# Optimization experiments

Hardware: AMD Instinct MI355X
Metric: run time of the kernel (lower is better)

The kernel has to match this reference:

```python
import jax, jax.numpy as jnp
import numpy as np

N, E = 100000, 1600000
D_IN, D_H, D_OUT = 128, 128, 64


def setup_inputs() -> dict:
    key = jax.random.key(0)
    ks = jax.random.split(key, 9)
    features = jax.random.normal(ks[0], (N, D_IN), dtype=jnp.float32)
    src = jax.random.randint(ks[1], (E,), 0, N, dtype=jnp.int32)
    dst = jax.random.randint(ks[2], (E,), 0, N, dtype=jnp.int32)
    # GraphConv weights (glorot-ish scale)
    W1 = jax.random.normal(ks[3], (D_IN, D_H), dtype=jnp.float32) * (1.0 / np.sqrt(D_IN))
    b1 = jnp.zeros((D_H,), dtype=jnp.float32)
    W2 = jax.random.normal(ks[4], (D_H, D_H), dtype=jnp.float32) * (1.0 / np.sqrt(D_H))
    b2 = jnp.zeros((D_H,), dtype=jnp.float32)
    W3 = jax.random.normal(ks[5], (D_H, D_OUT), dtype=jnp.float32) * (1.0 / np.sqrt(D_H))
    b3 = jnp.zeros((D_OUT,), dtype=jnp.float32)
    return {"features": features, "src": src, "dst": dst,
            "W1": W1, "b1": b1, "W2": W2, "b2": b2, "W3": W3, "b3": b3}


def reference(features, src, dst, W1, b1, W2, b2, W3, b3):
    n = features.shape[0]
    ones_e = jnp.ones(src.shape[0], dtype=features.dtype)
    # DGL GraphConv norm='both': degrees clamped to min 1
    out_deg = jnp.clip(jax.ops.segment_sum(ones_e, src, num_segments=n), 1.0)
    in_deg = jnp.clip(jax.ops.segment_sum(ones_e, dst, num_segments=n), 1.0)
    norm_src = out_deg ** -0.5  # [N]
    norm_dst = in_deg ** -0.5   # [N]

    def graph_conv(h, W, b, relu):
        h = h * norm_src[:, None]                                   # D_out^{-1/2} scale
        m = jax.ops.segment_sum(h[src], dst, num_segments=n)        # SpMM aggregate
        m = m * norm_dst[:, None]                                   # D_in^{-1/2} scale
        h = m @ W + b                                               # linear
        return jax.nn.relu(h) if relu else h

    # dropout is identity in eval mode (deterministic reference)
    h = graph_conv(features, W1, b1, True)
    h = graph_conv(h, W2, b2, True)
    h = graph_conv(h, W3, b3, False)
    return jax.nn.log_softmax(h, axis=1)
```

## Files before the change

### kernel.cpp

```cpp
#include <hip/hip_runtime.h>
#include <math.h>

#define D 128
#define DO 64

#define CHUNK_BITS 15
#define CHUNK_SZ   32768
#define HWORDS     (CHUNK_SZ/4)
#define NSLICE     64

typedef unsigned int uint32;
typedef short bf8s __attribute__((ext_vector_type(8)));
typedef float f32x16 __attribute__((ext_vector_type(16)));

__device__ __forceinline__ unsigned short f2bf(float f) {
    uint32 u = __float_as_uint(f);
    u += 0x7FFFu + ((u >> 16) & 1u);
    return (unsigned short)(u >> 16);
}
__device__ __forceinline__ float bf_lo(uint32 p) { return __uint_as_float(p << 16); }
__device__ __forceinline__ float bf_hi(uint32 p) { return __uint_as_float(p & 0xFFFF0000u); }
__device__ __forceinline__ void acc2(float4& a, uint2 q) {
    a.x += bf_lo(q.x); a.y += bf_hi(q.x);
    a.z += bf_lo(q.y); a.w += bf_hi(q.y);
}
__device__ __forceinline__ void accs(float4& a, uint2 q, float s) {
    a.x = fmaf(bf_lo(q.x), s, a.x); a.y = fmaf(bf_hi(q.x), s, a.y);
    a.z = fmaf(bf_lo(q.y), s, a.z); a.w = fmaf(bf_hi(q.y), s, a.w);
}

__device__ __forceinline__ f32x16 mfma32(bf8s a, bf8s b, f32x16 c) {
    return __builtin_amdgcn_mfma_f32_32x32x16_bf16(a, b, c, 0, 0, 0);
}
#define ZERO16 {0.f,0.f,0.f,0.f,0.f,0.f,0.f,0.f,0.f,0.f,0.f,0.f,0.f,0.f,0.f,0.f}

__global__ void k_pack_w(const float* __restrict__ W1, const float* __restrict__ W2,
                         const float* __restrict__ W3,
                         unsigned short* __restrict__ P1, unsigned short* __restrict__ P2,
                         unsigned short* __restrict__ P3) {
    int t = blockIdx.x * 256 + threadIdx.x;
    const float* W; unsigned short* P; int slot, NCT, ncols;
    if (t < 2048)      { W = W1; P = P1; slot = t;        NCT = 4; ncols = 128; }
    else if (t < 4096) { W = W2; P = P2; slot = t - 2048; NCT = 4; ncols = 128; }
    else if (t < 5120) { W = W3; P = P3; slot = t - 4096; NCT = 2; ncols = 64;  }
    else return;
    int lane = slot & 63, rest = slot >> 6;
    int ct = rest % NCT, ks = rest / NCT;
    int k0 = ks * 16 + (lane >> 5) * 8;
    int colidx = ct * 32 + (lane & 31);
    unsigned u[4];
#pragma unroll
    for (int b = 0; b < 4; ++b) {
        unsigned lo = f2bf(W[(size_t)(k0 + 2 * b) * ncols + colidx]);
        unsigned hi = f2bf(W[(size_t)(k0 + 2 * b + 1) * ncols + colidx]);
        u[b] = lo | (hi << 16);
    }
    ((uint4*)P)[slot] = make_uint4(u[0], u[1], u[2], u[3]);
}

__global__ __launch_bounds__(256) void k_hist_gemm1(
    const int* __restrict__ src, const int* __restrict__ dst, int E,
    int NH, int NBg, int gemmPer,
    uint32* __restrict__ histS, uint32* __restrict__ histD,
    const float* __restrict__ F, const unsigned short* __restrict__ Wp1,
    unsigned short* __restrict__ T1, int N) {
    __shared__ __align__(16) char smemraw[64 * 132 * 4];
    const int tid = threadIdx.x;
    const int P = 1 + gemmPer;
    const int per = blockIdx.x / P;
    const int pos = blockIdx.x % P;

    if (pos == 0) {
        if (per >= 2 * NH) return;
        bool isS = per >= NH;
        int h = isS ? per - NH : per;
        int chunk = h / NSLICE, slice = h % NSLICE;
        const int* key = isS ? src : dst;
        uint32* hist = (uint32*)smemraw;
        for (int w = tid; w < HWORDS; w += 256) hist[w] = 0;
        __syncthreads();
        int base = chunk << CHUNK_BITS;
        const int nE4 = E >> 2;
        int lo = (int)(((long long)slice * nE4) / NSLICE);
        int hi = (int)(((long long)(slice + 1) * nE4) / NSLICE);
        for (int idx = lo + tid; idx < hi; idx += 256) {
            int4 k4 = ((const int4*)key)[idx];
            unsigned o;
            o = (unsigned)(k4.x - base); if (o < CHUNK_SZ) atomicAdd(&hist[o >> 2], 1u << ((o & 3) * 8));
            o = (unsigned)(k4.y - base); if (o < CHUNK_SZ) atomicAdd(&hist[o >> 2], 1u << ((o & 3) * 8));
            o = (unsigned)(k4.z - base); if (o < CHUNK_SZ) atomicAdd(&hist[o >> 2], 1u << ((o & 3) * 8));
            o = (unsigned)(k4.w - base); if (o < CHUNK_SZ) atomicAdd(&hist[o >> 2], 1u << ((o & 3) * 8));
        }
        if (slice == NSLICE - 1 && tid == 0) {
            for (int i = nE4 * 4; i < E; ++i) {
                unsigned o = (unsigned)(key[i] - base);
                if (o < CHUNK_SZ) atomicAdd(&hist[o >> 2], 1u << ((o & 3) * 8));
            }
        }
        __syncthreads();
        uint32* outp = (isS ? histS : histD) + (size_t)h * HWORDS;
        for (int w = tid; w < HWORDS; w += 256) outp[w] = hist[w];
        return;
    }
    int gid = per * gemmPer + (pos - 1);
    if (gid >= NBg) return;
    const int n0 = gid * 64;
    const float4* M4 = (const float4*)F;
#pragma unroll
    for (int it = 0; it < 8; ++it) {
        int id = it * 256 + tid;
        int nl = id >> 5, k4 = id & 31;
        float4 v = make_float4(0.f, 0.f, 0.f, 0.f);
        int n = n0 + nl;
        if (n < N) v = M4[(size_t)n * 32 + k4];
        ushort4 o;
        o.x = f2bf(v.x); o.y = f2bf(v.y); o.z = f2bf(v.z); o.w = f2bf(v.w);
        *(ushort4*)(smemraw + ((unsigned)(nl * 256 + k4 * 8) ^ ((nl & 15) << 4))) = o;
    }
    __syncthreads();
    const int wid = tid >> 6, wl = tid & 63;
    const int rt = wid >> 1, ctb = (wid & 1) * 2;
    const bf8s* Wp = (const bf8s*)Wp1;
    f32x16 acc0 = ZERO16, acc1 = ZERO16;
    const int arow = rt * 32 + (wl & 31);
    const unsigned axor = (unsigned)((arow & 15) << 4);
    const unsigned abase = (unsigned)(arow * 256 + (wl >> 5) * 16);
#pragma unroll
    for (int ks = 0; ks < 8; ++ks) {
        bf8s af = *(const bf8s*)(smemraw + ((abase + ks * 32) ^ axor));
        acc0 = mfma32(af, Wp[(ks * 4 + ctb) * 64 + wl], acc0);
        acc1 = mfma32(af, Wp[(ks * 4 + ctb + 1) * 64 + wl], acc1);
    }
    const int colb = wl & 31;
    const int rbase = rt * 32 + ((wl >> 5) << 2);
#pragma unroll
    for (int reg = 0; reg < 16; ++reg) {
        int n = n0 + (reg & 3) + 8 * (reg >> 2) + rbase;
        if (n < N) {
            T1[(size_t)n * 128 + ctb * 32 + colb] = f2bf(acc0[reg]);
            T1[(size_t)n * 128 + (ctb + 1) * 32 + colb] = f2bf(acc1[reg]);
        }
    }
}

__global__ void k_merge_norms(const uint32* __restrict__ histS, uint32* __restrict__ histD,
                              int* __restrict__ degi, float* __restrict__ ns,
                              float* __restrict__ nd, int N, int NCHUNK) {
    int w = blockIdx.x * 256 + threadIdx.x;
    if (w >= NCHUNK * HWORDS) return;
    int chunk = w / HWORDS, ww = w - chunk * HWORDS;
    int n0 = (chunk << CHUNK_BITS) + ww * 4;
    if (n0 >= N) return;
    size_t basehist = ((size_t)chunk * NSLICE) * HWORDS + ww;
    uint32 runD = 0, runS = 0;
#pragma unroll 4
    for (int s = 0; s < NSLICE; ++s) {
        size_t idx = basehist + (size_t)s * HWORDS;
        uint32 c = histD[idx];
        histD[idx] = runD;
        runD += c;
        runS += histS[idx];
    }
#pragma unroll
    for (int k = 0; k < 4; ++k) {
        int n = n0 + k;
        if (n < N) {
            int dcur = (int)((runD >> (k * 8)) & 0xFF);
            int ocur = (int)((runS >> (k * 8)) & 0xFF);
            degi[n] = dcur;
            ns[n] = rsqrtf((float)(ocur < 1 ? 1 : ocur));
            nd[n] = rsqrtf((float)(dcur < 1 ? 1 : dcur));
        }
    }
}

__global__ void k_scan_block(const int* __restrict__ cnt, int* __restrict__ rp,
                             int* __restrict__ bsum, int N) {
    __shared__ int sdat[256];
    int i = blockIdx.x * 256 + threadIdx.x;
    int v = (i < N) ? cnt[i] : 0;
    sdat[threadIdx.x] = v;
    __syncthreads();
    for (int off = 1; off < 256; off <<= 1) {
        int t = (threadIdx.x >= off) ? sdat[threadIdx.x - off] : 0;
        __syncthreads();
        sdat[threadIdx.x] += t;
        __syncthreads();
    }
    if (i < N) rp[i] = sdat[threadIdx.x] - v;
    if (threadIdx.x == 255) bsum[blockIdx.x] = sdat[255];
}

__global__ void k_scan_add(int* __restrict__ rp, const int* __restrict__ bsum,
                           int N, int E, int NB,
                           uint32* __restrict__ Az, uint32* __restrict__ Bz,
                           float* __restrict__ nsN) {
    __shared__ int sred[256];
    const int b = blockIdx.x;
    const int tid = threadIdx.x;
    int v = 0;
    for (int k = tid; k < b; k += 256) v += bsum[k];
    sred[tid] = v;
    __syncthreads();
    for (int off = 128; off; off >>= 1) {
        if (tid < off) sred[tid] += sred[tid + off];
        __syncthreads();
    }
    int S = sred[0];
    int i = b * 256 + tid;
    if (i < N) rp[i] += S;
    if (i == N) rp[N] = E;
    if (i < 64) { Az[i] = 0; Bz[i] = 0; }
    if (b == 0 && tid == 0) nsN[0] = 0.f;
}

__global__ __launch_bounds__(256) void k_scatter(
    const int* __restrict__ src, const int* __restrict__ dst, int E,
    const uint32* __restrict__ histD, const int* __restrict__ rp,
    int* __restrict__ col) {
    __shared__ uint32 cnt[HWORDS];
    const int tid = threadIdx.x;
    int chunk = blockIdx.x / NSLICE, slice = blockIdx.x % NSLICE;
    const uint32* Pslice = histD + ((size_t)(chunk * NSLICE + slice)) * HWORDS;
    for (int w = tid; w < HWORDS; w += 256) cnt[w] = Pslice[w];
    __syncthreads();
    int base = chunk << CHUNK_BITS;
    const int nE4 = E >> 2;
    int lo = (int)(((long long)slice * nE4) / NSLICE);
    int hi = (int)(((long long)(slice + 1) * nE4) / NSLICE);
    for (int idx = lo + tid; idx < hi; idx += 256) {
        int4 s4 = ((const int4*)src)[idx];
        int4 d4 = ((const int4*)dst)[idx];
        unsigned o;
        o = (unsigned)(d4.x - base);
        if (o < CHUNK_SZ) {
            uint32 old = atomicAdd(&cnt[o >> 2], 1u << ((o & 3) * 8));
            col[rp[d4.x] + ((old >> ((o & 3) * 8)) & 0xFF)] = s4.x;
        }
        o = (unsigned)(d4.y - base);
        if (o < CHUNK_SZ) {
            uint32 old = atomicAdd(&cnt[o >> 2], 1u << ((o & 3) * 8));
            col[rp[d4.y] + ((old >> ((o & 3) * 8)) & 0xFF)] = s4.y;
        }
        o = (unsigned)(d4.z - base);
        if (o < CHUNK_SZ) {
            uint32 old = atomicAdd(&cnt[o >> 2], 1u << ((o & 3) * 8));
            col[rp[d4.z] + ((old >> ((o & 3) * 8)) & 0xFF)] = s4.z;
        }
        o = (unsigned)(d4.w - base);
        if (o < CHUNK_SZ) {
            uint32 old = atomicAdd(&cnt[o >> 2], 1u << ((o & 3) * 8));
            col[rp[d4.w] + ((old >> ((o & 3) * 8)) & 0xFF)] = s4.w;
        }
    }
    if (slice == NSLICE - 1 && tid == 0) {
        for (int i = nE4 * 4; i < E; ++i) {
            unsigned o = (unsigned)(dst[i] - base);
            if (o < CHUNK_SZ) {
                uint32 old = atomicAdd(&cnt[o >> 2], 1u << ((o & 3) * 8));
                col[rp[dst[i]] + ((old >> ((o & 3) * 8)) & 0xFF)] = src[i];
            }
        }
    }
}


#define SPMM_SH(K) int c##K = __shfl(cvec, j + K, 32);
#define SPMM_NS(K) float s##K = SC ? nsc[c##K] : 0.f;
#define SPMM_LD(K) uint2 q##K = T2[(((unsigned)c##K) << 5) + (unsigned)lane];
#define SPMM_AC(K) { if (SC) accs(((K) & 1) ? a1 : a0, q##K, s##K); \
                     else    acc2(((K) & 1) ? a1 : a0, q##K); }

template <bool SC>
__device__ __forceinline__ float4 spmm_gather_row(
    const uint2* __restrict__ T2, const int* __restrict__ col,
    const float* __restrict__ nsc,
    int s, int e, int cvec, int lane, int N) {
    float4 a0 = make_float4(0.f, 0.f, 0.f, 0.f), a1 = a0;
    int base = s, rem = e - s;
#pragma unroll 1
    while (rem > 0) {
        int cnt = rem < 32 ? rem : 32;
        int padded = (cnt + 7) & ~7;
        int j = 0;
#pragma unroll 1
        for (; j + 16 <= padded; j += 16) {
            SPMM_SH(0) SPMM_SH(1) SPMM_SH(2) SPMM_SH(3)
            SPMM_SH(4) SPMM_SH(5) SPMM_SH(6) SPMM_SH(7)
            SPMM_SH(8) SPMM_SH(9) SPMM_SH(10) SPMM_SH(11)
            SPMM_SH(12) SPMM_SH(13) SPMM_SH(14) SPMM_SH(15)
            SPMM_NS(0) SPMM_NS(1) SPMM_NS(2) SPMM_NS(3)
            SPMM_NS(4) SPMM_NS(5) SPMM_NS(6) SPMM_NS(7)
            SPMM_NS(8) SPMM_NS(9) SPMM_NS(10) SPMM_NS(11)
            SPMM_NS(12) SPMM_NS(13) SPMM_NS(14) SPMM_NS(15)
            SPMM_LD(0) SPMM_LD(1) SPMM_LD(2) SPMM_LD(3)
            SPMM_LD(4) SPMM_LD(5) SPMM_LD(6) SPMM_LD(7)
            SPMM_LD(8) SPMM_LD(9) SPMM_LD(10) SPMM_LD(11)
            SPMM_LD(12) SPMM_LD(13) SPMM_LD(14) SPMM_LD(15)
            SPMM_AC(0) SPMM_AC(1) SPMM_AC(2) SPMM_AC(3)
            SPMM_AC(4) SPMM_AC(5) SPMM_AC(6) SPMM_AC(7)
            SPMM_AC(8) SPMM_AC(9) SPMM_AC(10) SPMM_AC(11)
            SPMM_AC(12) SPMM_AC(13) SPMM_AC(14) SPMM_AC(15)
        }
        if (j < padded) {
            SPMM_SH(0) SPMM_SH(1) SPMM_SH(2) SPMM_SH(3)
            SPMM_SH(4) SPMM_SH(5) SPMM_SH(6) SPMM_SH(7)
            SPMM_NS(0) SPMM_NS(1) SPMM_NS(2) SPMM_NS(3)
            SPMM_NS(4) SPMM_NS(5) SPMM_NS(6) SPMM_NS(7)
            SPMM_LD(0) SPMM_LD(1) SPMM_LD(2) SPMM_LD(3)
            SPMM_LD(4) SPMM_LD(5) SPMM_LD(6) SPMM_LD(7)
            SPMM_AC(0) SPMM_AC(1) SPMM_AC(2) SPMM_AC(3)
            SPMM_AC(4) SPMM_AC(5) SPMM_AC(6) SPMM_AC(7)
        }
        base += 32; rem -= 32;
        if (rem > 0) {
            int t = base + lane;
            cvec = (t < e) ? col[t] : N;
        }
    }
    float4 r;
    r.x = a0.x + a1.x; r.y = a0.y + a1.y;
    r.z = a0.z + a1.z; r.w = a0.w + a1.w;
    return r;
}

#define A64_SH(K) int c##K = __shfl(cvec, j + K, 32);
#define A64_LD(K) uint32 q##K = Y2[(((size_t)(unsigned)c##K) << 5) + (unsigned)lane];
#define A64_AC(K) { if ((K) & 1) { lo1 += bf_lo(q##K); hi1 += bf_hi(q##K); } \
                    else         { lo0 += bf_lo(q##K); hi0 += bf_hi(q##K); } }

__device__ __forceinline__ float2 agg64_gather_row(
    const uint32* __restrict__ Y2, const int* __restrict__ col,
    int s, int e, int cvec, int lane, int N) {
    float lo0 = 0.f, hi0 = 0.f, lo1 = 0.f, hi1 = 0.f;
    int base = s, rem = e - s;
#pragma unroll 1
    while (rem > 0) {
        int cnt = rem < 32 ? rem : 32;
        int padded = (cnt + 7) & ~7;
        int j = 0;
#pragma unroll 1
        for (; j + 16 <= padded; j += 16) {
            A64_SH(0) A64_SH(1) A64_SH(2) A64_SH(3)
            A64_SH(4) A64_SH(5) A64_SH(6) A64_SH(7)
            A64_SH(8) A64_SH(9) A64_SH(10) A64_SH(11)
            A64_SH(12) A64_SH(13) A64_SH(14) A64_SH(15)
            A64_LD(0) A64_LD(1) A64_LD(2) A64_LD(3)
            A64_LD(4) A64_LD(5) A64_LD(6) A64_LD(7)
            A64_LD(8) A64_LD(9) A64_LD(10) A64_LD(11)
            A64_LD(12) A64_LD(13) A64_LD(14) A64_LD(15)
            A64_AC(0) A64_AC(1) A64_AC(2) A64_AC(3)
            A64_AC(4) A64_AC(5) A64_AC(6) A64_AC(7)
            A64_AC(8) A64_AC(9) A64_AC(10) A64_AC(11)
            A64_AC(12) A64_AC(13) A64_AC(14) A64_AC(15)
        }
        if (j < padded) {
            A64_SH(0) A64_SH(1) A64_SH(2) A64_SH(3)
            A64_SH(4) A64_SH(5) A64_SH(6) A64_SH(7)
            A64_LD(0) A64_LD(1) A64_LD(2) A64_LD(3)
            A64_LD(4) A64_LD(5) A64_LD(6) A64_LD(7)
            A64_AC(0) A64_AC(1) A64_AC(2) A64_AC(3)
            A64_AC(4) A64_AC(5) A64_AC(6) A64_AC(7)
        }
        base += 32; rem -= 32;
        if (rem > 0) {
            int t = base + lane;
            cvec = (t < e) ? col[t] : N;
        }
    }
    return make_float2(lo0 + lo1, hi0 + hi1);
}

template <int JOUT, bool SC>
__global__ __launch_bounds__(256) void k_spmm_gemm(
    const unsigned short* __restrict__ T, const int* __restrict__ rp,
    const int* __restrict__ col, const float* __restrict__ ns,
    const float* __restrict__ nd, const float* __restrict__ bias,
    const unsigned short* __restrict__ Wpk, unsigned short* __restrict__ out, int N) {
    __shared__ __align__(16) char MsRaw[32 * 256];
    if (JOUT == 64 && blockIdx.x == 0 && threadIdx.x < 32) {
        ((uint32*)out)[(size_t)N * 32 + threadIdx.x] = 0;
    }
    const int n0 = blockIdx.x * 32;
    const int g = threadIdx.x >> 5;
    const int lane = threadIdx.x & 31;
    const uint2* T2 = (const uint2*)T;
    float4 bv = ((const float4*)bias)[lane];

    const int row0 = n0 + (g << 2);
    int rb = 0;
    {
        int idx = row0 + lane;
        if (idx > N) idx = N;
        if (lane < 5) rb = rp[idx];
    }
    int s0 = __shfl(rb, 0, 32), s1 = __shfl(rb, 1, 32), s2 = __shfl(rb, 2, 32),
        s3 = __shfl(rb, 3, 32), s4 = __shfl(rb, 4, 32);
    int cv0 = N, cv1 = N, cv2 = N, cv3 = N;
    { int t = s0 + lane; if (t < s1) cv0 = col[t]; }
    { int t = s1 + lane; if (t < s2) cv1 = col[t]; }
    { int t = s2 + lane; if (t < s3) cv2 = col[t]; }
    { int t = s3 + lane; if (t < s4) cv3 = col[t]; }

#define SPMM_ROW_EPI(RI, SS, EE, CV) { \
    float4 t = spmm_gather_row<SC>(T2, col, ns, SS, EE, CV, lane, N); \
    int row = row0 + RI; \
    if (row < N) { \
        float sd = nd[row], sr = ns[row]; \
        ushort4 o; \
        o.x = f2bf(fmaxf(fmaf(t.x, sd, bv.x), 0.f) * sr); \
        o.y = f2bf(fmaxf(fmaf(t.y, sd, bv.y), 0.f) * sr); \
        o.z = f2bf(fmaxf(fmaf(t.z, sd, bv.z), 0.f) * sr); \
        o.w = f2bf(fmaxf(fmaf(t.w, sd, bv.w), 0.f) * sr); \
        int lr = row - n0; \
        *(ushort4*)(MsRaw + ((unsigned)(lr * 256 + lane * 8) ^ ((lr & 15) << 4))) = o; \
    } }

    SPMM_ROW_EPI(0, s0, s1, cv0)
    SPMM_ROW_EPI(1, s1, s2, cv1)
    SPMM_ROW_EPI(2, s2, s3, cv2)
    SPMM_ROW_EPI(3, s3, s4, cv3)
#undef SPMM_ROW_EPI

    __syncthreads();
    const int wid = threadIdx.x >> 6, wl = threadIdx.x & 63;
    const int NCT = (JOUT == 128) ? 4 : 2;
    if (JOUT == 128 || wid < 2) {
        const bf8s* Wp = (const bf8s*)Wpk;
        f32x16 acc = ZERO16;
        const int arow = wl & 31;
        const unsigned axor = (unsigned)((arow & 15) << 4);
        const unsigned abase = (unsigned)(arow * 256 + (wl >> 5) * 16);
#pragma unroll
        for (int ks = 0; ks < 8; ++ks) {
            bf8s af = *(const bf8s*)(MsRaw + ((abase + ks * 32) ^ axor));
            acc = mfma32(af, Wp[(ks * NCT + wid) * 64 + wl], acc);
        }
        const int colb = wid * 32 + (wl & 31);
        const int rb2 = (wl >> 5) << 2;
#pragma unroll
        for (int reg = 0; reg < 16; ++reg) {
            int n = n0 + (reg & 3) + 8 * (reg >> 2) + rb2;
            if (n < N) out[(size_t)n * JOUT + colb] = f2bf(acc[reg]);
        }
    }
}

__global__ __launch_bounds__(256) void k_agg64_lsm(
    const unsigned short* __restrict__ Y, const int* __restrict__ rp,
    const int* __restrict__ col, const float* __restrict__ nd,
    const float* __restrict__ b3, float* __restrict__ out, int N) {
    int row = blockIdx.x * 8 + (threadIdx.x >> 5);
    if (row >= N) return;
    int lane = threadIdx.x & 31;
    const uint32* Y2 = (const uint32*)Y;
    int s = rp[row], e = rp[row + 1];
    int cv;
    { int t = s + lane; cv = (t < e) ? col[t] : N; }
    float2 agg = agg64_gather_row(Y2, col, s, e, cv, lane, N);
    float sd = nd[row];
    float2 bb = ((const float2*)b3)[lane];
    float v0 = agg.x * sd + bb.x;
    float v1 = agg.y * sd + bb.y;
    float m = fmaxf(v0, v1);
#pragma unroll
    for (int o = 16; o; o >>= 1) m = fmaxf(m, __shfl_xor(m, o, 32));
    float ex = expf(v0 - m) + expf(v1 - m);
#pragma unroll
    for (int o = 16; o; o >>= 1) ex += __shfl_xor(ex, o, 32);
    float ls = m + logf(ex);
    ((float2*)out)[(size_t)row * 32 + lane] = make_float2(v0 - ls, v1 - ls);
}

extern "C" void kernel_launch(void* const* d_in, const int* in_sizes, int n_in,
                              void* d_out, int out_size, void* d_ws, size_t ws_size,
                              hipStream_t stream) {
    const float* features = (const float*)d_in[0];
    const int*   src      = (const int*)d_in[1];
    const int*   dst      = (const int*)d_in[2];
    const float* W1       = (const float*)d_in[3];
    const float* b1       = (const float*)d_in[4];
    const float* W2       = (const float*)d_in[5];
    const float* b2       = (const float*)d_in[6];
    const float* W3       = (const float*)d_in[7];
    const float* b3       = (const float*)d_in[8];
    float* out = (float*)d_out;

    const int N = in_sizes[0] / D;
    const int E = in_sizes[1];

    const int NCHUNK = (N + CHUNK_SZ - 1) >> CHUNK_BITS;
    const int NH = NCHUNK * NSLICE;

    char* p = (char*)d_ws;
    unsigned short* A = (unsigned short*)p; p += ((size_t)N + 1) * D * sizeof(unsigned short);
    unsigned short* B = (unsigned short*)p; p += ((size_t)N + 1) * D * sizeof(unsigned short);
    int* col    = (int*)p;   p += (size_t)E * sizeof(int);
    int* rp     = (int*)p;   p += ((size_t)N + 4) * sizeof(int);
    int* degi   = (int*)p;   p += (size_t)N * sizeof(int);
    float* ns   = (float*)p; p += ((size_t)N + 4) * sizeof(float);
    float* nd   = (float*)p; p += (size_t)N * sizeof(float);
    int* bsum   = (int*)p;   p += 4096 * sizeof(int);
    uint32* histS = (uint32*)p; p += (size_t)NH * HWORDS * sizeof(uint32);
    uint32* histD = (uint32*)p; p += (size_t)NH * HWORDS * sizeof(uint32);
    unsigned short* Wp1 = (unsigned short*)p; p += 16384 * sizeof(unsigned short);
    unsigned short* Wp2 = (unsigned short*)p; p += 16384 * sizeof(unsigned short);
    unsigned short* Wp3 = (unsigned short*)p; p += 8192 * sizeof(unsigned short);

    const int gN  = (N + 255) / 256;
    const int NBg = (N + 63) / 64;
    const int periods = 2 * NH;
    const int gemmPer = (NBg + periods - 1) / periods;
    const int G1 = periods * (1 + gemmPer);

    k_pack_w<<<20, 256, 0, stream>>>(W1, W2, W3, Wp1, Wp2, Wp3);
    k_hist_gemm1<<<G1, 256, 0, stream>>>(src, dst, E, NH, NBg, gemmPer,
                                         histS, histD, features, Wp1, B, N);
    k_merge_norms<<<(NCHUNK * HWORDS + 255) / 256, 256, 0, stream>>>(
        histS, histD, degi, ns, nd, N, NCHUNK);
    k_scan_block<<<gN, 256, 0, stream>>>(degi, rp, bsum, N);
    k_scan_add<<<(N + 1 + 255) / 256, 256, 0, stream>>>(
        rp, bsum, N, E, gN,
        (uint32*)(A + (size_t)N * D), (uint32*)(B + (size_t)N * D), ns + N);
    k_scatter<<<NH, 256, 0, stream>>>(src, dst, E, histD, rp, col);

    const int NBn32 = (N + 31) / 32;
    k_spmm_gemm<128, true><<<NBn32, 256, 0, stream>>>(B, rp, col, ns, nd, b1, Wp2, A, N);
    k_spmm_gemm<64, false><<<NBn32, 256, 0, stream>>>(A, rp, col, ns, nd, b2, Wp3, B, N);
    k_agg64_lsm<<<(N + 7) / 8, 256, 0, stream>>>(B, rp, col, nd, b3, out, N);
}
```

Measured before the change: 340.7 us.

## Fold source norm into GEMM1 output, fuse GEMM1 with scatter, widen histogram

The GEMM1 blocks move from the histogram kernel to the scatter kernel, where the source-degree norm is already known. That norm is applied to T1 in the GEMM epilogue, so the first SpMM no longer gathers ns per edge. The histogram kernel now covers two 32K chunks per block with a 64 KB LDS histogram across 256 fixed blocks. This cuts the number of passes over the edge arrays. In exchange, the GEMM no longer overlaps the histogram, and the larger LDS footprint lowers occupancy; the 256-block grid also assumes four chunks.

Result: slower. 417.7 us (+22.6%).

```diff
diff --git a/kernel.cpp b/kernel.cpp
--- a/kernel.cpp
+++ b/kernel.cpp
@@ -23,10 +23,6 @@
 __device__ __forceinline__ void acc2(float4& a, uint2 q) {
     a.x += bf_lo(q.x); a.y += bf_hi(q.x);
     a.z += bf_lo(q.y); a.w += bf_hi(q.y);
-}
-__device__ __forceinline__ void accs(float4& a, uint2 q, float s) {
-    a.x = fmaf(bf_lo(q.x), s, a.x); a.y = fmaf(bf_hi(q.x), s, a.y);
-    a.z = fmaf(bf_lo(q.y), s, a.z); a.w = fmaf(bf_hi(q.y), s, a.w);
 }
 
 __device__ __forceinline__ f32x16 mfma32(bf8s a, bf8s b, f32x16 c) {
@@ -58,88 +54,40 @@
     ((uint4*)P)[slot] = make_uint4(u[0], u[1], u[2], u[3]);
 }
 
-__global__ __launch_bounds__(256) void k_hist_gemm1(
+__global__ __launch_bounds__(256) void k_hist2(
     const int* __restrict__ src, const int* __restrict__ dst, int E,
-    int NH, int NBg, int gemmPer,
-    uint32* __restrict__ histS, uint32* __restrict__ histD,
-    const float* __restrict__ F, const unsigned short* __restrict__ Wp1,
-    unsigned short* __restrict__ T1, int N) {
-    __shared__ __align__(16) char smemraw[64 * 132 * 4];
+    uint32* __restrict__ histS, uint32* __restrict__ histD) {
+    __shared__ uint32 hist[2 * HWORDS];
     const int tid = threadIdx.x;
-    const int P = 1 + gemmPer;
-    const int per = blockIdx.x / P;
-    const int pos = blockIdx.x % P;
-
-    if (pos == 0) {
-        if (per >= 2 * NH) return;
-        bool isS = per >= NH;
-        int h = isS ? per - NH : per;
-        int chunk = h / NSLICE, slice = h % NSLICE;
-        const int* key = isS ? src : dst;
-        uint32* hist = (uint32*)smemraw;
-        for (int w = tid; w < HWORDS; w += 256) hist[w] = 0;
-        __syncthreads();
-        int base = chunk << CHUNK_BITS;
-        const int nE4 = E >> 2;
-        int lo = (int)(((long long)slice * nE4) / NSLICE);
-        int hi = (int)(((long long)(slice + 1) * nE4) / NSLICE);
-        for (int idx = lo + tid; idx < hi; idx += 256) {
-            int4 k4 = ((const int4*)key)[idx];
-            unsigned o;
-            o = (unsigned)(k4.x - base); if (o < CHUNK_SZ) atomicAdd(&hist[o >> 2], 1u << ((o & 3) * 8));
-            o = (unsigned)(k4.y - base); if (o < CHUNK_SZ) atomicAdd(&hist[o >> 2], 1u << ((o & 3) * 8));
-            o = (unsigned)(k4.z - base); if (o < CHUNK_SZ) atomicAdd(&hist[o >> 2], 1u << ((o & 3) * 8));
-            o = (unsigned)(k4.w - base); if (o < CHUNK_SZ) atomicAdd(&hist[o >> 2], 1u << ((o & 3) * 8));
-        }
-        if (slice == NSLICE - 1 && tid == 0) {
-            for (int i = nE4 * 4; i < E; ++i) {
-                unsigned o = (unsigned)(key[i] - base);
-                if (o < CHUNK_SZ) atomicAdd(&hist[o >> 2], 1u << ((o & 3) * 8));
-            }
-        }
-        __syncthreads();
-        uint32* outp = (isS ? histS : histD) + (size_t)h * HWORDS;
-        for (int w = tid; w < HWORDS; w += 256) outp[w] = hist[w];
-        return;
-    }
-    int gid = per * gemmPer + (pos - 1);
-    if (gid >= NBg) return;
-    const int n0 = gid * 64;
-    const float4* M4 = (const float4*)F;
-#pragma unroll
-    for (int it = 0; it < 8; ++it) {
-        int id = it * 256 + tid;
-        int nl = id >> 5, k4 = id & 31;
-        float4 v = make_float4(0.f, 0.f, 0.f, 0.f);
-        int n = n0 + nl;
-        if (n < N) v = M4[(size_t)n * 32 + k4];
-        ushort4 o;
-        o.x = f2bf(v.x); o.y = f2bf(v.y); o.z = f2bf(v.z); o.w = f2bf(v.w);
-        *(ushort4*)(smemraw + ((unsigned)(nl * 256 + k4 * 8) ^ ((nl & 15) << 4))) = o;
-    }
+    const bool isS = blockIdx.x >= 128;
+    const int rest = blockIdx.x & 127;
+    const int pair = rest >> 6, slice = rest & 63;
+    const int* key = isS ? src : dst;
+    for (int w = tid; w < 2 * HWORDS; w += 256) hist[w] = 0;
     __syncthreads();
-    const int wid = tid >> 6, wl = tid & 63;
-    const int rt = wid >> 1, ctb = (wid & 1) * 2;
-    const bf8s* Wp = (const bf8s*)Wp1;
-    f32x16 acc0 = ZERO16, acc1 = ZERO16;
-    const int arow = rt * 32 + (wl & 31);
-    const unsigned axor = (unsigned)((arow & 15) << 4);
-    const unsigned abase = (unsigned)(arow * 256 + (wl >> 5) * 16);
-#pragma unroll
-    for (int ks = 0; ks < 8; ++ks) {
-        bf8s af = *(const bf8s*)(smemraw + ((abase + ks * 32) ^ axor));
-        acc0 = mfma32(af, Wp[(ks * 4 + ctb) * 64 + wl], acc0);
-        acc1 = mfma32(af, Wp[(ks * 4 + ctb + 1) * 64 + wl], acc1);
-    }
-    const int colb = wl & 31;
-    const int rbase = rt * 32 + ((wl >> 5) << 2);
-#pragma unroll
-    for (int reg = 0; reg < 16; ++reg) {
-        int n = n0 + (reg & 3) + 8 * (reg >> 2) + rbase;
-        if (n < N) {
-            T1[(size_t)n * 128 + ctb * 32 + colb] = f2bf(acc0[reg]);
-            T1[(size_t)n * 128 + (ctb + 1) * 32 + colb] = f2bf(acc1[reg]);
-        }
+    const int base = pair << 16;
+    const int nE4 = E >> 2;
+    int lo = (int)(((long long)slice * nE4) / NSLICE);
+    int hi = (int)(((long long)(slice + 1) * nE4) / NSLICE);
+    for (int idx = lo + tid; idx < hi; idx += 256) {
+        int4 k4 = ((const int4*)key)[idx];
+        unsigned o;
+        o = (unsigned)(k4.x - base); if (o < 2 * CHUNK_SZ) atomicAdd(&hist[o >> 2], 1u << ((o & 3) * 8));
+        o = (unsigned)(k4.y - base); if (o < 2 * CHUNK_SZ) atomicAdd(&hist[o >> 2], 1u << ((o & 3) * 8));
+        o = (unsigned)(k4.z - base); if (o < 2 * CHUNK_SZ) atomicAdd(&hist[o >> 2], 1u << ((o & 3) * 8));
+        o = (unsigned)(k4.w - base); if (o < 2 * CHUNK_SZ) atomicAdd(&hist[o >> 2], 1u << ((o & 3) * 8));
+    }
+    if (slice == NSLICE - 1 && tid == 0) {
+        for (int i = nE4 * 4; i < E; ++i) {
+            unsigned o = (unsigned)(key[i] - base);
+            if (o < 2 * CHUNK_SZ) atomicAdd(&hist[o >> 2], 1u << ((o & 3) * 8));
+        }
+    }
+    __syncthreads();
+    uint32* outp = isS ? histS : histD;
+    for (int w = tid; w < 2 * HWORDS; w += 256) {
+        int chunk = (pair << 1) + (w >> 13);
+        outp[((size_t)(chunk * NSLICE + slice)) * HWORDS + (w & (HWORDS - 1))] = hist[w];
     }
 }
 
@@ -192,9 +140,8 @@
 }
 
 __global__ void k_scan_add(int* __restrict__ rp, const int* __restrict__ bsum,
-                           int N, int E, int NB,
-                           uint32* __restrict__ Az, uint32* __restrict__ Bz,
-                           float* __restrict__ nsN) {
+                           int N, int E,
+                           uint32* __restrict__ Az, uint32* __restrict__ Bz) {
     __shared__ int sred[256];
     const int b = blockIdx.x;
     const int tid = threadIdx.x;
@@ -211,70 +158,116 @@
     if (i < N) rp[i] += S;
     if (i == N) rp[N] = E;
     if (i < 64) { Az[i] = 0; Bz[i] = 0; }
-    if (b == 0 && tid == 0) nsN[0] = 0.f;
-}
-
-__global__ __launch_bounds__(256) void k_scatter(
+}
+
+__global__ __launch_bounds__(256) void k_scatter_gemm1(
     const int* __restrict__ src, const int* __restrict__ dst, int E,
+    int NH, int NBg, int gemmPer,
     const uint32* __restrict__ histD, const int* __restrict__ rp,
-    int* __restrict__ col) {
-    __shared__ uint32 cnt[HWORDS];
+    int* __restrict__ col,
+    const float* __restrict__ F, const unsigned short* __restrict__ Wp1,
+    const float* __restrict__ ns, unsigned short* __restrict__ T1, int N) {
+    __shared__ __align__(16) char smemraw[64 * 132 * 4];
     const int tid = threadIdx.x;
-    int chunk = blockIdx.x / NSLICE, slice = blockIdx.x % NSLICE;
-    const uint32* Pslice = histD + ((size_t)(chunk * NSLICE + slice)) * HWORDS;
-    for (int w = tid; w < HWORDS; w += 256) cnt[w] = Pslice[w];
-    __syncthreads();
-    int base = chunk << CHUNK_BITS;
-    const int nE4 = E >> 2;
-    int lo = (int)(((long long)slice * nE4) / NSLICE);
-    int hi = (int)(((long long)(slice + 1) * nE4) / NSLICE);
-    for (int idx = lo + tid; idx < hi; idx += 256) {
-        int4 s4 = ((const int4*)src)[idx];
-        int4 d4 = ((const int4*)dst)[idx];
-        unsigned o;
-        o = (unsigned)(d4.x - base);
-        if (o < CHUNK_SZ) {
-            uint32 old = atomicAdd(&cnt[o >> 2], 1u << ((o & 3) * 8));
-            col[rp[d4.x] + ((old >> ((o & 3) * 8)) & 0xFF)] = s4.x;
-        }
-        o = (unsigned)(d4.y - base);
-        if (o < CHUNK_SZ) {
-            uint32 old = atomicAdd(&cnt[o >> 2], 1u << ((o & 3) * 8));
-            col[rp[d4.y] + ((old >> ((o & 3) * 8)) & 0xFF)] = s4.y;
-        }
-        o = (unsigned)(d4.z - base);
-        if (o < CHUNK_SZ) {
-            uint32 old = atomicAdd(&cnt[o >> 2], 1u << ((o & 3) * 8));
-            col[rp[d4.z] + ((old >> ((o & 3) * 8)) & 0xFF)] = s4.z;
-        }
-        o = (unsigned)(d4.w - base);
-        if (o < CHUNK_SZ) {
-            uint32 old = atomicAdd(&cnt[o >> 2], 1u << ((o & 3) * 8));
-            col[rp[d4.w] + ((old >> ((o & 3) * 8)) & 0xFF)] = s4.w;
-        }
-    }
-    if (slice == NSLICE - 1 && tid == 0) {
-        for (int i = nE4 * 4; i < E; ++i) {
-            unsigned o = (unsigned)(dst[i] - base);
+    const int P = 1 + gemmPer;
+    const int per = blockIdx.x / P;
+    const int pos = blockIdx.x % P;
+
+    if (pos == 0) {
+        uint32* cnt = (uint32*)smemraw;
+        int chunk = per / NSLICE, slice = per % NSLICE;
+        const uint32* Pslice = histD + ((size_t)(chunk * NSLICE + slice)) * HWORDS;
+        for (int w = tid; w < HWORDS; w += 256) cnt[w] = Pslice[w];
+        __syncthreads();
+        int base = chunk << CHUNK_BITS;
+        const int nE4 = E >> 2;
+        int lo = (int)(((long long)slice * nE4) / NSLICE);
+        int hi = (int)(((long long)(slice + 1) * nE4) / NSLICE);
+        for (int idx = lo + tid; idx < hi; idx += 256) {
+            int4 s4 = ((const int4*)src)[idx];
+            int4 d4 = ((const int4*)dst)[idx];
+            unsigned o;
+            o = (unsigned)(d4.x - base);
             if (o < CHUNK_SZ) {
                 uint32 old = atomicAdd(&cnt[o >> 2], 1u << ((o & 3) * 8));
-                col[rp[dst[i]] + ((old >> ((o & 3) * 8)) & 0xFF)] = src[i];
+                col[rp[d4.x] + ((old >> ((o & 3) * 8)) & 0xFF)] = s4.x;
             }
+            o = (unsigned)(d4.y - base);
+            if (o < CHUNK_SZ) {
+                uint32 old = atomicAdd(&cnt[o >> 2], 1u << ((o & 3) * 8));
+                col[rp[d4.y] + ((old >> ((o & 3) * 8)) & 0xFF)] = s4.y;
+            }
+            o = (unsigned)(d4.z - base);
+            if (o < CHUNK_SZ) {
+                uint32 old = atomicAdd(&cnt[o >> 2], 1u << ((o & 3) * 8));
+                col[rp[d4.z] + ((old >> ((o & 3) * 8)) & 0xFF)] = s4.z;
+            }
+            o = (unsigned)(d4.w - base);
+            if (o < CHUNK_SZ) {
+                uint32 old = atomicAdd(&cnt[o >> 2], 1u << ((o & 3) * 8));
+                col[rp[d4.w] + ((old >> ((o & 3) * 8)) & 0xFF)] = s4.w;
+            }
+        }
+        if (slice == NSLICE - 1 && tid == 0) {
+            for (int i = nE4 * 4; i < E; ++i) {
+                unsigned o = (unsigned)(dst[i] - base);
+                if (o < CHUNK_SZ) {
+                    uint32 old = atomicAdd(&cnt[o >> 2], 1u << ((o & 3) * 8));
+                    col[rp[dst[i]] + ((old >> ((o & 3) * 8)) & 0xFF)] = src[i];
+                }
+            }
+        }
+        return;
+    }
+    int gid = per * gemmPer + (pos - 1);
+    if (gid >= NBg) return;
+    const int n0 = gid * 64;
+    const float4* M4 = (const float4*)F;
+#pragma unroll
+    for (int it = 0; it < 8; ++it) {
+        int id = it * 256 + tid;
+        int nl = id >> 5, k4 = id & 31;
+        float4 v = make_float4(0.f, 0.f, 0.f, 0.f);
+        int n = n0 + nl;
+        if (n < N) v = M4[(size_t)n * 32 + k4];
+        ushort4 o;
+        o.x = f2bf(v.x); o.y = f2bf(v.y); o.z = f2bf(v.z); o.w = f2bf(v.w);
+        *(ushort4*)(smemraw + ((unsigned)(nl * 256 + k4 * 8) ^ ((nl & 15) << 4))) = o;
+    }
+    __syncthreads();
+    const int wid = tid >> 6, wl = tid & 63;
+    const int rt = wid >> 1, ctb = (wid & 1) * 2;
+    const bf8s* Wp = (const bf8s*)Wp1;
+    f32x16 acc0 = ZERO16, acc1 = ZERO16;
+    const int arow = rt * 32 + (wl & 31);
+    const unsigned axor = (unsigned)((arow & 15) << 4);
+    const unsigned abase = (unsigned)(arow * 256 + (wl >> 5) * 16);
+#pragma unroll
+    for (int ks = 0; ks < 8; ++ks) {
+        bf8s af = *(const bf8s*)(smemraw + ((abase + ks * 32) ^ axor));
+        acc0 = mfma32(af, Wp[(ks * 4 + ctb) * 64 + wl], acc0);
+        acc1 = mfma32(af, Wp[(ks * 4 + ctb + 1) * 64 + wl], acc1);
+    }
+    const int colb = wl & 31;
+    const int rbase = rt * 32 + ((wl >> 5) << 2);
+#pragma unroll
+    for (int reg = 0; reg < 16; ++reg) {
+        int n = n0 + (reg & 3) + 8 * (reg >> 2) + rbase;
+        if (n < N) {
+            float sn = ns[n];
+            T1[(size_t)n * 128 + ctb * 32 + colb] = f2bf(acc0[reg] * sn);
+            T1[(size_t)n * 128 + (ctb + 1) * 32 + colb] = f2bf(acc1[reg] * sn);
         }
     }
 }
 
 
 #define SPMM_SH(K) int c##K = __shfl(cvec, j + K, 32);
-#define SPMM_NS(K) float s##K = SC ? nsc[c##K] : 0.f;
 #define SPMM_LD(K) uint2 q##K = T2[(((unsigned)c##K) << 5) + (unsigned)lane];
-#define SPMM_AC(K) { if (SC) accs(((K) & 1) ? a1 : a0, q##K, s##K); \
-                     else    acc2(((K) & 1) ? a1 : a0, q##K); }
-
-template <bool SC>
+#define SPMM_AC(K) acc2(((K) & 1) ? a1 : a0, q##K);
+
 __device__ __forceinline__ float4 spmm_gather_row(
     const uint2* __restrict__ T2, const int* __restrict__ col,
-    const float* __restrict__ nsc,
     int s, int e, int cvec, int lane, int N) {
     float4 a0 = make_float4(0.f, 0.f, 0.f, 0.f), a1 = a0;
     int base = s, rem = e - s;
@@ -289,10 +282,6 @@
             SPMM_SH(4) SPMM_SH(5) SPMM_SH(6) SPMM_SH(7)
             SPMM_SH(8) SPMM_SH(9) SPMM_SH(10) SPMM_SH(11)
             SPMM_SH(12) SPMM_SH(13) SPMM_SH(14) SPMM_SH(15)
-            SPMM_NS(0) SPMM_NS(1) SPMM_NS(2) SPMM_NS(3)
-            SPMM_NS(4) SPMM_NS(5) SPMM_NS(6) SPMM_NS(7)
-            SPMM_NS(8) SPMM_NS(9) SPMM_NS(10) SPMM_NS(11)
-            SPMM_NS(12) SPMM_NS(13) SPMM_NS(14) SPMM_NS(15)
             SPMM_LD(0) SPMM_LD(1) SPMM_LD(2) SPMM_LD(3)
             SPMM_LD(4) SPMM_LD(5) SPMM_LD(6) SPMM_LD(7)
             SPMM_LD(8) SPMM_LD(9) SPMM_LD(10) SPMM_LD(11)
@@ -305,8 +294,6 @@
         if (j < padded) {
             SPMM_SH(0) SPMM_SH(1) SPMM_SH(2) SPMM_SH(3)
             SPMM_SH(4) SPMM_SH(5) SPMM_SH(6) SPMM_SH(7)
-            SPMM_NS(0) SPMM_NS(1) SPMM_NS(2) SPMM_NS(3)
-            SPMM_NS(4) SPMM_NS(5) SPMM_NS(6) SPMM_NS(7)
             SPMM_LD(0) SPMM_LD(1) SPMM_LD(2) SPMM_LD(3)
             SPMM_LD(4) SPMM_LD(5) SPMM_LD(6) SPMM_LD(7)
             SPMM_AC(0) SPMM_AC(1) SPMM_AC(2) SPMM_AC(3)
@@ -371,7 +358,7 @@
     return make_float2(lo0 + lo1, hi0 + hi1);
 }
 
-template <int JOUT, bool SC>
+template <int JOUT>
 __global__ __launch_bounds__(256) void k_spmm_gemm(
     const unsigned short* __restrict__ T, const int* __restrict__ rp,
     const int* __restrict__ col, const float* __restrict__ ns,
@@ -403,7 +390,7 @@
     { int t = s3 + lane; if (t < s4) cv3 = col[t]; }
 
 #define SPMM_ROW_EPI(RI, SS, EE, CV) { \
-    float4 t = spmm_gather_row<SC>(T2, col, ns, SS, EE, CV, lane, N); \
+    float4 t = spmm_gather_row(T2, col, SS, EE, CV, lane, N); \
     int row = row0 + RI; \
     if (row < N) { \
         float sd = nd[row], sr = ns[row]; \
@@ -498,7 +485,7 @@
     int* col    = (int*)p;   p += (size_t)E * sizeof(int);
     int* rp     = (int*)p;   p += ((size_t)N + 4) * sizeof(int);
     int* degi   = (int*)p;   p += (size_t)N * sizeof(int);
-    float* ns   = (float*)p; p += ((size_t)N + 4) * sizeof(float);
+    float* ns   = (float*)p; p += (size_t)N * sizeof(float);
     float* nd   = (float*)p; p += (size_t)N * sizeof(float);
     int* bsum   = (int*)p;   p += 4096 * sizeof(int);
     uint32* histS = (uint32*)p; p += (size_t)NH * HWORDS * sizeof(uint32);
@@ -509,23 +496,22 @@
 
     const int gN  = (N + 255) / 256;
     const int NBg = (N + 63) / 64;
-    const int periods = 2 * NH;
-    const int gemmPer = (NBg + periods - 1) / periods;
-    const int G1 = periods * (1 + gemmPer);
+    const int gemmPer = (NBg + NH - 1) / NH;
+    const int G1 = NH * (1 + gemmPer);
 
     k_pack_w<<<20, 256, 0, stream>>>(W1, W2, W3, Wp1, Wp2, Wp3);
-    k_hist_gemm1<<<G1, 256, 0, stream>>>(src, dst, E, NH, NBg, gemmPer,
-                                         histS, histD, features, Wp1, B, N);
+    k_hist2<<<256, 256, 0, stream>>>(src, dst, E, histS, histD);
     k_merge_norms<<<(NCHUNK * HWORDS + 255) / 256, 256, 0, stream>>>(
         histS, histD, degi, ns, nd, N, NCHUNK);
     k_scan_block<<<gN, 256, 0, stream>>>(degi, rp, bsum, N);
     k_scan_add<<<(N + 1 + 255) / 256, 256, 0, stream>>>(
-        rp, bsum, N, E, gN,
-        (uint32*)(A + (size_t)N * D), (uint32*)(B + (size_t)N * D), ns + N);
-    k_scatter<<<NH, 256, 0, stream>>>(src, dst, E, histD, rp, col);
+        rp, bsum, N, E,
+        (uint32*)(A + (size_t)N * D), (uint32*)(B + (size_t)N * D));
+    k_scatter_gemm1<<<G1, 256, 0, stream>>>(src, dst, E, NH, NBg, gemmPer,
+                                            histD, rp, col, features, Wp1, ns, B, N);
 
     const int NBn32 = (N + 31) / 32;
-    k_spmm_gemm<128, true><<<NBn32, 256, 0, stream>>>(B, rp, col, ns, nd, b1, Wp2, A, N);
-    k_spmm_gemm<64, false><<<NBn32, 256, 0, stream>>>(A, rp, col, ns, nd, b2, Wp3, B, N);
+    k_spmm_gemm<128><<<NBn32, 256, 0, stream>>>(B, rp, col, ns, nd, b1, Wp2, A, N);
+    k_spmm_gemm<64><<<NBn32, 256, 0, stream>>>(A, rp, col, ns, nd, b2, Wp3, B, N);
     k_agg64_lsm<<<(N + 7) / 8, 256, 0, stream>>>(B, rp, col, nd, b3, out, N);
 }
```
